# Kernel tuning notes

Hardware: AMD Instinct MI355X
Metric: run time of the kernel (lower is better)

The kernel has to match this reference:

```python
import jax, jax.numpy as jnp
import numpy as np

N_WORDS = 4096
N_HEADS = 512
EMB = 768          # input_size
HID = 1024         # hidden_size
DIST = 64          # dist_emb_size (forced by Conv1d(64, ...))
SENT_LEN = 64      # fixed sentence length -> static max padded length
PAIR_F = 2 * EMB + DIST  # 1600


def setup_inputs() -> dict:
    key = jax.random.key(0)
    ks = jax.random.split(key, 14)
    words = jax.random.normal(ks[0], (N_WORDS, EMB), dtype=jnp.float32)
    heads_ids = jax.random.randint(ks[1], (N_HEADS,), 0, N_WORDS, dtype=jnp.int64)
    sent_id = (jnp.arange(N_WORDS) // SENT_LEN).astype(jnp.int32)  # sorted, contiguous sentences
    s = 0.02
    return {
        "words": words,
        "heads_ids": heads_ids,
        "sent_id": sent_id,
        "emb_table": jax.random.normal(ks[2], (128, DIST), dtype=jnp.float32) * s,
        "W1": jax.random.normal(ks[3], (PAIR_F, HID), dtype=jnp.float32) * s,
        "b1": jnp.zeros((HID,), jnp.float32),
        "W2": jax.random.normal(ks[4], (HID, 256), dtype=jnp.float32) * s,
        "b2": jnp.zeros((256,), jnp.float32),
        "W3": jax.random.normal(ks[5], (256, DIST), dtype=jnp.float32) * s,
        "b3": jnp.zeros((DIST,), jnp.float32),
        "cw1": jax.random.normal(ks[6], (4, DIST, 3), dtype=jnp.float32) * s,  # Conv1d(64,4,3,1,1)
        "cb1": jnp.zeros((4,), jnp.float32),
        "cw2": jax.random.normal(ks[7], (2, 4, 3), dtype=jnp.float32) * s,    # Conv1d(4,2,3,1,1)
        "cb2": jnp.zeros((2,), jnp.float32),
    }


def _conv1d(x, w, b):
    # x: [N, C_in, L], w: [C_out, C_in, 3], padding=1, stride=1 (torch Conv1d semantics)
    y = jax.lax.conv_general_dilated(x, w, window_strides=(1,), padding=((1, 1),),
                                     dimension_numbers=("NCH", "OIH", "NCH"))
    return y + b[None, :, None]


def reference(words, heads_ids, sent_id, emb_table, W1, b1, W2, b2, W3, b3, cw1, cb1, cw2, cb2):
    n_words = words.shape[0]
    heads = heads_ids.astype(jnp.int32)
    H = heads.shape[0]

    # relative positions & distance-embedding ids, clamped to bucket 127 outside [-63, 63]
    rel = heads[:, None] - jnp.arange(n_words, dtype=jnp.int32)[None, :]      # [H, W]
    eid = rel + 63
    eid = jnp.where((eid < 0) | (eid > 126), 127, eid)

    # per-head sentence span (sent_id is sorted & contiguous)
    sh = sent_id[heads]
    starts = jnp.searchsorted(sent_id, sh, side="left")
    lengths = jnp.searchsorted(sent_id, sh, side="right") - starts            # [H]

    # padded ragged layout: row i holds words of head i's sentence, left-packed
    j = jnp.arange(SENT_LEN, dtype=jnp.int32)
    cols = starts[:, None] + j[None, :]                                       # [H, L]
    mask = j[None, :] < lengths[:, None]                                      # [H, L]
    cols_c = jnp.clip(cols, 0, n_words - 1)

    head_w = words[heads]                                                     # [H, E]
    col_w = words[cols_c]                                                     # [H, L, E]
    dist = emb_table[jnp.take_along_axis(eid, cols_c, axis=1)]                # [H, L, DIST]
    feat = jnp.concatenate(
        [jnp.broadcast_to(head_w[:, None, :], col_w.shape), col_w, dist], axis=-1)
    feat = jnp.where(mask[..., None], feat, jnp.zeros((), feat.dtype))        # zero padding rows (as torch)

    # FFNN (dropout is identity in eval mode)
    x = jax.nn.relu(feat @ W1 + b1)
    x = jax.nn.relu(x @ W2 + b2)
    x = x @ W3 + b3                                                           # [H, L, 64]

    # conv stack over the padded ragged axis
    x = _conv1d(x.transpose(0, 2, 1), cw1, cb1)
    x = _conv1d(x, cw2, cb2)
    res = x.transpose(0, 2, 1)                                                # [H, L, 2]

    # scatter back into [H, n_words, 2]; masked slots get out-of-range col -> dropped
    rows = jnp.broadcast_to(jnp.arange(H, dtype=jnp.int32)[:, None], mask.shape)
    cols_sc = jnp.where(mask, cols, n_words)
    scores = jnp.full((H, n_words, 2), -jnp.inf, dtype=words.dtype)
    scores = scores.at[rows, cols_sc].set(res, mode="drop")

    # eval-mode validity log-mask
    valid_starts = jnp.log((rel >= 0).astype(words.dtype))
    valid_ends = jnp.log((rel <= 0).astype(words.dtype))
    valid = jnp.stack([valid_starts, valid_ends], axis=2)
    return scores + valid
```

## Files before the change

kernel.cpp:

```cpp
#include <hip/hip_runtime.h>
#include <math.h>

#define NW   4096
#define NH   512
#define EMBD 768
#define HIDD 1024
#define DISTD 64
#define SLEN 64

#define NEG_BIG (-1.0e30f)

typedef __attribute__((ext_vector_type(8))) short short8;
typedef __attribute__((ext_vector_type(16))) float f32x16;
typedef __attribute__((ext_vector_type(4))) float f32x4;

#define MFMA32(a, b, c) __builtin_amdgcn_mfma_f32_32x32x16_bf16((a), (b), (c), 0, 0, 0)
#define MFMA16(a, b, c) __builtin_amdgcn_mfma_f32_16x16x32_bf16((a), (b), (c), 0, 0, 0)

__device__ __forceinline__ unsigned short f2bf(float f) {
    unsigned u = __float_as_uint(f);
    u += 0x7FFFu + ((u >> 16) & 1u);
    return (unsigned short)(u >> 16);
}
__device__ __forceinline__ float bf2f(unsigned short s) {
    return __uint_as_float(((unsigned)s) << 16);
}
__device__ __forceinline__ unsigned cvtpk(float lo, float hi) {
    unsigned r;
    asm("v_cvt_pk_bf16_f32 %0, %1, %2" : "=v"(r) : "v"(lo), "v"(hi));
    return r;
}
__device__ __forceinline__ short8 pack8(float f0, float f1, float f2, float f3,
                                        float f4, float f5, float f6, float f7) {
    union { unsigned u[4]; short8 s; } r;
    r.u[0] = cvtpk(f0, f1); r.u[1] = cvtpk(f2, f3);
    r.u[2] = cvtpk(f4, f5); r.u[3] = cvtpk(f6, f7);
    return r.s;
}

#define BARL()                                                   \
    do {                                                         \
        asm volatile("s_waitcnt lgkmcnt(0)" ::: "memory");       \
        __builtin_amdgcn_s_barrier();                            \
    } while (0)

__device__ __forceinline__ void pack_b32_dev(long t, const float* __restrict__ src,
                                             int ld, int nb32, int KB,
                                             unsigned short* __restrict__ dst)
{
    int l = (int)(t & 63); long u = t >> 6;
    int nb = (int)(u % nb32); int kb = (int)(u / nb32);
    int row0 = kb * 16 + ((l >> 5) << 3);
    int col  = (nb << 5) + (l & 31);
    const float* s = src + (size_t)row0 * ld + col;
    short8 v;
#pragma unroll
    for (int j = 0; j < 8; ++j) v[j] = (short)f2bf(s[(size_t)j * ld]);
    *(short8*)(dst + (((size_t)nb * KB + kb) << 9) + l * 8) = v;
}

__device__ __forceinline__ void pack_b16_dev(long t, const float* __restrict__ src,
                                             int ld, int nb16, int KB,
                                             unsigned short* __restrict__ dst)
{
    int l = (int)(t & 63); long u = t >> 6;
    int nb = (int)(u % nb16); int kb = (int)(u / nb16);
    int row0 = kb * 32 + ((l >> 4) << 3);
    int col  = (nb << 4) + (l & 15);
    const float* s = src + (size_t)row0 * ld + col;
    short8 v;
#pragma unroll
    for (int j = 0; j < 8; ++j) v[j] = (short)f2bf(s[(size_t)j * ld]);
    *(short8*)(dst + (((size_t)nb * KB + kb) << 9) + l * 8) = v;
}

__device__ __forceinline__ void cvt8_dev(long i, const float* __restrict__ src,
                                         unsigned short* __restrict__ dst)
{
    const float* s = src + i * 8;
    short8 v;
#pragma unroll
    for (int j = 0; j < 8; ++j) v[j] = (short)f2bf(s[j]);
    *(short8*)(dst + i * 8) = v;
}

#define WPS 776
__global__ __launch_bounds__(256)
void prep_kernel(const float* __restrict__ words, const float* __restrict__ emb,
                 const float* __restrict__ W1,
                 unsigned short* __restrict__ wpack, unsigned short* __restrict__ embb,
                 unsigned short* __restrict__ W1pa, unsigned short* __restrict__ W1px,
                 unsigned short* __restrict__ W1pd)
{
    __shared__ unsigned short tls[32 * WPS];

    const int b = blockIdx.x, tid = threadIdx.x;
    if (b < 128) {
        const int m = b;
#pragma unroll
        for (int i = 0; i < 24; ++i) {
            const int idx = tid + i * 256;
            const int r = idx / 192, c4 = (idx % 192) * 4;
            float4 v = *(const float4*)(words + ((size_t)(m * 32 + r)) * EMBD + c4);
            tls[r * WPS + c4 + 0] = f2bf(v.x);
            tls[r * WPS + c4 + 1] = f2bf(v.y);
            tls[r * WPS + c4 + 2] = f2bf(v.z);
            tls[r * WPS + c4 + 3] = f2bf(v.w);
        }
        __syncthreads();
        const int l = tid & 63, w = tid >> 6;
        for (int kb = w; kb < 48; kb += 4) {
            short8 v = *(const short8*)&tls[(l & 31) * WPS + kb * 16 + ((l >> 5) << 3)];
            *(short8*)(wpack + (((size_t)m * 48 + kb) << 9) + l * 8) = v;
        }
    } else if (b < 132) {
        cvt8_dev((long)(b - 128) * 256 + tid, emb, embb);
    } else if (b < 516) {
        pack_b32_dev((long)(b - 132) * 256 + tid, W1, HIDD, 32, 48, W1pa);
    } else if (b < 900) {
        pack_b32_dev((long)(b - 516) * 256 + tid, W1 + (size_t)768 * HIDD, HIDD, 32, 48, W1px);
    } else {
        pack_b32_dev((long)(b - 900) * 256 + tid, W1 + (size_t)1536 * HIDD, HIDD, 32, 4, W1pd);
    }
}

__global__ __launch_bounds__(256, 4)
void gemms_kernel(const unsigned short* __restrict__ wpack,
                  const unsigned short* __restrict__ embb,
                  const unsigned short* __restrict__ W1pa,
                  const unsigned short* __restrict__ W1px,
                  const unsigned short* __restrict__ W1pd,
                  const float* __restrict__ W2, const float* __restrict__ W3,
                  const float* __restrict__ b1, const int* __restrict__ heads,
                  const int* __restrict__ sent_id,
                  unsigned short* __restrict__ XwP, unsigned short* __restrict__ Hcb,
                  unsigned short* __restrict__ Dtb,
                  unsigned short* __restrict__ W2p, unsigned short* __restrict__ W3p,
                  int* __restrict__ starts, int* __restrict__ lens)
{
    __shared__ unsigned short tls[4][32 * 40];

    const int b = blockIdx.x, tid = threadIdx.x;
    const int l = tid & 63, w = tid >> 6;

    if (b < 1024) {
        const int mB = b >> 3, nB = b & 7;
        const int cbg = nB * 4 + w;
        const unsigned short* ap = wpack + (((size_t)mB * 48) << 9) + l * 8;
        const unsigned short* bp = W1px + (((size_t)cbg * 48) << 9) + l * 8;
        f32x16 acc = {};
#pragma unroll
        for (int kk = 0; kk < 48; ++kk) {
            short8 a = *(const short8*)(ap + ((size_t)kk << 9));
            short8 bb = *(const short8*)(bp + ((size_t)kk << 9));
            acc = MFMA32(a, bb, acc);
        }
        const int col = cbg * 32 + (l & 31);
        const float bv = b1[col];
        unsigned short* tw = tls[w];
#pragma unroll
        for (int r = 0; r < 16; ++r) {
            int rowl = (r & 3) + 8 * (r >> 2) + 4 * (l >> 5);
            tw[rowl * 40 + (l & 31)] = f2bf(acc[r] + bv);
        }
        short8 v0 = *(const short8*)&tw[(l & 31) * 40 + ((l >> 5) << 3)];
        short8 v1 = *(const short8*)&tw[(l & 31) * 40 + 16 + ((l >> 5) << 3)];
        *(short8*)(XwP + (((size_t)(mB * 64 + cbg * 2)) << 9) + l * 8) = v0;
        *(short8*)(XwP + (((size_t)(mB * 64 + cbg * 2 + 1)) << 9) + l * 8) = v1;
    } else if (b < 1152) {
        const int q = b - 1024;
        const int mB = q >> 3, nB = q & 7;
        const int cbg = nB * 4 + w;
        int row = heads[mB * 32 + (l & 31)];
        const unsigned short* ap = wpack + (((size_t)(row >> 5) * 48) << 9)
                                 + ((row & 31) + 32 * (l >> 5)) * 8;
        const unsigned short* bp = W1pa + (((size_t)cbg * 48) << 9) + l * 8;
        f32x16 acc = {};
#pragma unroll
        for (int kk = 0; kk < 48; ++kk) {
            short8 a = *(const short8*)(ap + ((size_t)kk << 9));
            short8 bb = *(const short8*)(bp + ((size_t)kk << 9));
            acc = MFMA32(a, bb, acc);
        }
        const int col = cbg * 32 + (l & 31);
#pragma unroll
        for (int r = 0; r < 16; ++r) {
            int rr = mB * 32 + (r & 3) + 8 * (r >> 2) + 4 * (l >> 5);
            Hcb[(size_t)rr * HIDD + col] = f2bf(acc[r]);
        }
    } else if (b < 1184) {
        const int q = b - 1152;
        const int mB = q >> 3, nB = q & 7;
        const int cbg = nB * 4 + w;
        const unsigned short* ap = embb + (size_t)(mB * 32 + (l & 31)) * DISTD + ((l >> 5) << 3);
        const unsigned short* bp = W1pd + (((size_t)cbg * 4) << 9) + l * 8;
        f32x16 acc = {};
#pragma unroll
        for (int kk = 0; kk < 4; ++kk) {
            short8 a = *(const short8*)(ap + kk * 16);
            short8 bb = *(const short8*)(bp + ((size_t)kk << 9));
            acc = MFMA32(a, bb, acc);
        }
        const int col = cbg * 32 + (l & 31);
#pragma unroll
        for (int r = 0; r < 16; ++r) {
            int rr = mB * 32 + (r & 3) + 8 * (r >> 2) + 4 * (l >> 5);
            Dtb[(size_t)rr * HIDD + col] = f2bf(acc[r]);
        }
    } else if (b < 1312) {
        pack_b32_dev((long)(b - 1184) * 256 + tid, W2, 256, 8, 64, W2p);
    } else if (b < 1320) {
        pack_b16_dev((long)(b - 1312) * 256 + tid, W3, 64, 4, 8, W3p);
    } else {
        int h = (b - 1320) * 256 + tid;
        if (h < NH) {
            int head = heads[h];
            int s = sent_id[head];
            int lo = 0, hi = NW;
            while (lo < hi) { int mid = (lo + hi) >> 1; if (sent_id[mid] < s) lo = mid + 1; else hi = mid; }
            int start = lo;
            lo = 0; hi = NW;
            while (lo < hi) { int mid = (lo + hi) >> 1; if (sent_id[mid] <= s) lo = mid + 1; else hi = mid; }
            int len = lo - start;
            if (len > SLEN) len = SLEN;
            starts[h] = start;
            lens[h] = len;
        }
    }
}

#define NT 32
__global__ __launch_bounds__(512)
void head_kernel(const unsigned short* __restrict__ XwP,
                 const unsigned short* __restrict__ Hcb,
                 const unsigned short* __restrict__ Dtb,
                 const unsigned short* __restrict__ W2p,
                 const float* __restrict__ b2,
                 const unsigned short* __restrict__ W3p,
                 const float* __restrict__ b3,
                 const float* __restrict__ cw1, const float* __restrict__ cb1,
                 const float* __restrict__ cw2, const float* __restrict__ cb2,
                 const int* __restrict__ heads, const int* __restrict__ starts,
                 const int* __restrict__ lens,
                 float* __restrict__ out)
{
    __shared__ char smem[67584];
    unsigned short* Ast = (unsigned short*)smem;
    unsigned short* Bst = (unsigned short*)(smem + 16384);
    unsigned short* x2s = (unsigned short*)smem;
    float* x3s = (float*)smem;
    float* y1s = (float*)(smem + 35328);
    float* y2s = (float*)(smem + 37376);

    const int tid = threadIdx.x;
    const int l = tid & 63, w = tid >> 6;
    const int h0 = blockIdx.x * 2;

    const int head0 = heads[h0],  head1 = heads[h0 + 1];
    const int strt0 = starts[h0], strt1 = starts[h0 + 1];
    const int len0  = lens[h0],   len1  = lens[h0 + 1];

    const int kkA = w >> 2, rb = w & 3;
    const int hbA = rb >> 1;
    const int headA = hbA ? head1 : head0;
    const int strtA = hbA ? strt1 : strt0;
    const int q0A = 63 - (headA - strtA);
    const unsigned short* xwPp =
        XwP + (((size_t)((strtA >> 5) + (rb & 1)) * 64) << 9) + l * 8;
    const int ddRow = 126 - q0A - 32 * (rb & 1) - (l & 31);
    const unsigned short* ddPp = Dtb + (size_t)ddRow * HIDD + ((l >> 5) << 3);
    const unsigned short* hcp = Hcb + (size_t)(h0 + hbA) * HIDD + ((l >> 5) << 3);
    const int kkB = w >> 2, nbB0 = (w & 3) * 2;
    const int mb = w & 1, nq = w >> 1;

    f32x16 acc[2][2] = {};

    short8 rxw, rhc, rdd, rb0, rb1;

#define LOADT(t)                                                              \
    {                                                                         \
        const int kb_ = (t) * 2 + kkA;                                        \
        rxw = *(const short8*)(xwPp + ((size_t)kb_ << 9));                    \
        rdd = *(const short8*)(ddPp + kb_ * 16);                              \
        rhc = *(const short8*)(hcp + kb_ * 16);                               \
        const size_t c0_ = ((size_t)(nbB0 * 64 + (t) * 2 + kkB)) << 9;        \
        rb0 = *(const short8*)(W2p + c0_ + l * 8);                            \
        rb1 = *(const short8*)(W2p + c0_ + 32768 + l * 8);                    \
    }

#define WRITET(t)                                                             \
    {                                                                         \
        const int buf_ = (t) & 1;                                             \
        float f_[8];                                                          \
        _Pragma("unroll")                                                     \
        for (int j = 0; j < 8; ++j)                                           \
            f_[j] = fmaxf(bf2f((unsigned short)rxw[j])                        \
                        + bf2f((unsigned short)rhc[j])                        \
                        + bf2f((unsigned short)rdd[j]), 0.f);                 \
        short8 v_ = pack8(f_[0], f_[1], f_[2], f_[3], f_[4], f_[5], f_[6], f_[7]); \
        *(short8*)&Ast[buf_ * 4096 + (kkA * 4 + rb) * 512 + l * 8] = v_;      \
        *(short8*)&Bst[buf_ * 8192 + (kkB * 8 + nbB0) * 512 + l * 8] = rb0;   \
        *(short8*)&Bst[buf_ * 8192 + (kkB * 8 + nbB0 + 1) * 512 + l * 8] = rb1; \
    }

    LOADT(0);
    WRITET(0);
    LOADT(1);
    BARL();

#pragma unroll 2
    for (int t = 0; t < NT; ++t) {
        const int buf = t & 1;
        short8 af0[2], af1[2], bf0[2], bf1[2];
#pragma unroll
        for (int k2 = 0; k2 < 2; ++k2) {
            af0[k2] = *(const short8*)&Ast[buf * 4096 + (k2 * 4 + mb * 2 + 0) * 512 + l * 8];
            af1[k2] = *(const short8*)&Ast[buf * 4096 + (k2 * 4 + mb * 2 + 1) * 512 + l * 8];
            bf0[k2] = *(const short8*)&Bst[buf * 8192 + (k2 * 8 + nq * 2 + 0) * 512 + l * 8];
            bf1[k2] = *(const short8*)&Bst[buf * 8192 + (k2 * 8 + nq * 2 + 1) * 512 + l * 8];
        }
        if (t + 1 < NT) WRITET(t + 1);
        if (t + 2 < NT) LOADT(t + 2);
#pragma unroll
        for (int k2 = 0; k2 < 2; ++k2) {
            acc[0][0] = MFMA32(af0[k2], bf0[k2], acc[0][0]);
            acc[0][1] = MFMA32(af0[k2], bf1[k2], acc[0][1]);
            acc[1][0] = MFMA32(af1[k2], bf0[k2], acc[1][0]);
            acc[1][1] = MFMA32(af1[k2], bf1[k2], acc[1][1]);
        }
        BARL();
    }

#pragma unroll
    for (int i = 0; i < 2; ++i) {
#pragma unroll
        for (int n = 0; n < 2; ++n) {
            const int ct = nq * 64 + n * 32 + (l & 31);
            const float bv = b2[ct];
#pragma unroll
            for (int r = 0; r < 16; ++r) {
                const int rt = mb * 64 + i * 32 + (r & 3) + 8 * (r >> 2) + 4 * (l >> 5);
                const int hb = rt >> 6, rl = rt & 63;
                x2s[hb * 16896 + rl * 264 + ct] = f2bf(fmaxf(acc[i][n][r] + bv, 0.f));
            }
        }
    }
    __syncthreads();

    {
        const int hb = w >> 2, q = w & 3;
        const unsigned short* x2h = x2s + hb * 16896;
        f32x4 acc2[4] = {};
#pragma unroll
        for (int kk = 0; kk < 8; ++kk) {
            short8 bf = *(const short8*)(W3p + ((q * 8 + kk) << 9) + l * 8);
#pragma unroll
            for (int mi = 0; mi < 4; ++mi) {
                short8 af = *(const short8*)&x2h[(mi * 16 + (l & 15)) * 264 + kk * 32 + ((l >> 4) << 3)];
                acc2[mi] = MFMA16(af, bf, acc2[mi]);
            }
        }
        __syncthreads();
        float* x3h = x3s + hb * 4416;
        const int col = q * 16 + (l & 15);
        const float b3v = b3[col];
#pragma unroll
        for (int mi = 0; mi < 4; ++mi) {
#pragma unroll
            for (int r = 0; r < 4; ++r) {
                const int rowv = mi * 16 + (l >> 4) * 4 + r;
                x3h[rowv * 69 + col] = acc2[mi][r] + b3v;
            }
        }
    }
    __syncthreads();

    {
        const int hb3 = tid >> 8;
        const int co = (tid >> 6) & 3;
        const int ll = tid & 63;
        const float* x3h = x3s + hb3 * 4416;
        float s = cb1[co];
        const float* wb = cw1 + co * DISTD * 3;
        for (int ci = 0; ci < DISTD; ++ci) {
            float w0 = wb[ci * 3 + 0], w1 = wb[ci * 3 + 1], w2v = wb[ci * 3 + 2];
            float xm = (ll > 0) ? x3h[(ll - 1) * 69 + ci] : 0.f;
            float xc = x3h[ll * 69 + ci];
            float xp = (ll < 63) ? x3h[(ll + 1) * 69 + ci] : 0.f;
            s = fmaf(xm, w0, s);
            s = fmaf(xc, w1, s);
            s = fmaf(xp, w2v, s);
        }
        y1s[hb3 * 256 + co * 64 + ll] = s;
    }
    __syncthreads();

    if (tid < 256) {
        const int hb4 = tid >> 7;
        const int co = (tid >> 6) & 1;
        const int ll = tid & 63;
        const float* yh = y1s + hb4 * 256;
        const int head = hb4 ? head1 : head0;
        const int strt = hb4 ? strt1 : strt0;
        float s = cb2[co];
#pragma unroll
        for (int ci = 0; ci < 4; ++ci) {
            const float* wb = cw2 + (co * 4 + ci) * 3;
            const float* yr = yh + ci * 64;
            float xm = (ll > 0) ? yr[ll - 1] : 0.f;
            float xc = yr[ll];
            float xp = (ll < 63) ? yr[ll + 1] : 0.f;
            s = fmaf(xm, wb[0], s);
            s = fmaf(xc, wb[1], s);
            s = fmaf(xp, wb[2], s);
        }
        const int col = strt + ll;
        const int rel = head - col;
        const bool valid = (co == 0) ? (rel >= 0) : (rel <= 0);
        y2s[hb4 * 128 + ll * 2 + co] = valid ? s : NEG_BIG;
    }
    __syncthreads();

    {
        const int hb = tid >> 8;
        const int c8 = tid & 255;
        const int strt = hb ? strt1 : strt0;
        const int len  = hb ? len1  : len0;
        float* orow = out + ((size_t)(h0 + hb) * NW) * 2;
        const float* yh = y2s + hb * 128;
#pragma unroll
        for (int i = 0; i < 16; ++i) {
            const int col = i * 256 + c8;
            float2 v;
            if (col >= strt && col < strt + len) {
                v = *(const float2*)&yh[(col - strt) * 2];
            } else {
                v.x = NEG_BIG; v.y = NEG_BIG;
            }
            *(float2*)&orow[(size_t)col * 2] = v;
        }
    }
}

extern "C" void kernel_launch(void* const* d_in, const int* in_sizes, int n_in,
                              void* d_out, int out_size, void* d_ws, size_t ws_size,
                              hipStream_t stream)
{
    const float* words = (const float*)d_in[0];
    const int* heads   = (const int*)d_in[1];
    const int* sent_id = (const int*)d_in[2];
    const float* emb   = (const float*)d_in[3];
    const float* W1    = (const float*)d_in[4];
    const float* b1    = (const float*)d_in[5];
    const float* W2    = (const float*)d_in[6];
    const float* b2    = (const float*)d_in[7];
    const float* W3    = (const float*)d_in[8];
    const float* b3    = (const float*)d_in[9];
    const float* cw1   = (const float*)d_in[10];
    const float* cb1   = (const float*)d_in[11];
    const float* cw2   = (const float*)d_in[12];
    const float* cb2   = (const float*)d_in[13];
    float* out = (float*)d_out;

    char* wsb = (char*)d_ws;
    unsigned short* XwP  = (unsigned short*)(wsb + 0);
    unsigned short* Hcb  = (unsigned short*)(wsb + 8388608);
    unsigned short* Dtb  = (unsigned short*)(wsb + 9437184);
    unsigned short* W2p  = (unsigned short*)(wsb + 9699328);
    unsigned short* W3p  = (unsigned short*)(wsb + 10223616);
    unsigned short* embb = (unsigned short*)(wsb + 10256384);
    int* starts          = (int*)(wsb + 10272768);
    int* lens            = (int*)(wsb + 10274816);
    char* ob = (char*)d_out;
    unsigned short* wpack  = (unsigned short*)(ob + 0);
    unsigned short* W1pa   = (unsigned short*)(ob + 6291456);
    unsigned short* W1px   = (unsigned short*)(ob + 7864320);
    unsigned short* W1pd   = (unsigned short*)(ob + 9437184);
    (void)ws_size; (void)in_sizes; (void)n_in; (void)out_size;

    prep_kernel<<<dim3(932), dim3(256), 0, stream>>>(
        words, emb, W1, wpack, embb, W1pa, W1px, W1pd);

    gemms_kernel<<<dim3(1322), dim3(256), 0, stream>>>(
        wpack, embb, W1pa, W1px, W1pd, W2, W3, b1, heads, sent_id,
        XwP, Hcb, Dtb, W2p, W3p, starts, lens);

    head_kernel<<<dim3(NH / 2), dim3(512), 0, stream>>>(
        XwP, Hcb, Dtb, W2p, b2, W3p, b3, cw1, cb1, cw2, cb2,
        heads, starts, lens, out);
}
```

Measured before the change: 73.67 us.

## Load W2 fragments directly into registers instead of staging through LDS

The W2 operand of the second GEMM is now read from global memory straight into per-wave register fragments, double-buffered two k-steps ahead, instead of being cooperatively loaded, written to shared memory and read back. This removes the LDS writes and reads for B and halves the shared-memory traffic per tile. In exchange, each wave fetches its own B fragments, so warps sharing the same columns load redundant copies from global/L2, and more registers are held live for the prefetched fragments.

```diff
diff --git a/kernel.cpp b/kernel.cpp
--- a/kernel.cpp
+++ b/kernel.cpp
@@ -246,7 +246,6 @@
 {
     __shared__ char smem[67584];
     unsigned short* Ast = (unsigned short*)smem;
-    unsigned short* Bst = (unsigned short*)(smem + 16384);
     unsigned short* x2s = (unsigned short*)smem;
     float* x3s = (float*)smem;
     float* y1s = (float*)(smem + 35328);
@@ -270,25 +269,25 @@
     const int ddRow = 126 - q0A - 32 * (rb & 1) - (l & 31);
     const unsigned short* ddPp = Dtb + (size_t)ddRow * HIDD + ((l >> 5) << 3);
     const unsigned short* hcp = Hcb + (size_t)(h0 + hbA) * HIDD + ((l >> 5) << 3);
-    const int kkB = w >> 2, nbB0 = (w & 3) * 2;
     const int mb = w & 1, nq = w >> 1;
+    const unsigned short* bp0 = W2p + (((size_t)(nq * 2) * 64) << 9) + l * 8;
+    const unsigned short* bp1 = W2p + (((size_t)(nq * 2 + 1) * 64) << 9) + l * 8;
 
     f32x16 acc[2][2] = {};
 
-    short8 rxw, rhc, rdd, rb0, rb1;
-
-#define LOADT(t)                                                              \
+    short8 rxw, rhc, rdd;
+    short8 sA00, sA01, sA10, sA11;
+    short8 sB00, sB01, sB10, sB11;
+
+#define LOADA(t)                                                              \
     {                                                                         \
         const int kb_ = (t) * 2 + kkA;                                        \
         rxw = *(const short8*)(xwPp + ((size_t)kb_ << 9));                    \
         rdd = *(const short8*)(ddPp + kb_ * 16);                              \
         rhc = *(const short8*)(hcp + kb_ * 16);                               \
-        const size_t c0_ = ((size_t)(nbB0 * 64 + (t) * 2 + kkB)) << 9;        \
-        rb0 = *(const short8*)(W2p + c0_ + l * 8);                            \
-        rb1 = *(const short8*)(W2p + c0_ + 32768 + l * 8);                    \
-    }
-
-#define WRITET(t)                                                             \
+    }
+
+#define WRITEA(t)                                                             \
     {                                                                         \
         const int buf_ = (t) & 1;                                             \
         float f_[8];                                                          \
@@ -299,35 +298,50 @@
                         + bf2f((unsigned short)rdd[j]), 0.f);                 \
         short8 v_ = pack8(f_[0], f_[1], f_[2], f_[3], f_[4], f_[5], f_[6], f_[7]); \
         *(short8*)&Ast[buf_ * 4096 + (kkA * 4 + rb) * 512 + l * 8] = v_;      \
-        *(short8*)&Bst[buf_ * 8192 + (kkB * 8 + nbB0) * 512 + l * 8] = rb0;   \
-        *(short8*)&Bst[buf_ * 8192 + (kkB * 8 + nbB0 + 1) * 512 + l * 8] = rb1; \
-    }
-
-    LOADT(0);
-    WRITET(0);
-    LOADT(1);
+    }
+
+#define LOADB(t, B00, B01, B10, B11)                                          \
+    {                                                                         \
+        const int kb0_ = (t) * 2;                                             \
+        B00 = *(const short8*)(bp0 + ((size_t)kb0_ << 9));                    \
+        B01 = *(const short8*)(bp1 + ((size_t)kb0_ << 9));                    \
+        B10 = *(const short8*)(bp0 + ((size_t)(kb0_ + 1) << 9));              \
+        B11 = *(const short8*)(bp1 + ((size_t)(kb0_ + 1) << 9));              \
+    }
+
+#define MFMA_STEP(buf_, B00, B01, B10, B11)                                   \
+    {                                                                         \
+        short8 af0_0 = *(const short8*)&Ast[(buf_) * 4096 + (mb * 2 + 0) * 512 + l * 8]; \
+        short8 af1_0 = *(const short8*)&Ast[(buf_) * 4096 + (mb * 2 + 1) * 512 + l * 8]; \
+        short8 af0_1 = *(const short8*)&Ast[(buf_) * 4096 + (4 + mb * 2 + 0) * 512 + l * 8]; \
+        short8 af1_1 = *(const short8*)&Ast[(buf_) * 4096 + (4 + mb * 2 + 1) * 512 + l * 8]; \
+        acc[0][0] = MFMA32(af0_0, B00, acc[0][0]);                            \
+        acc[0][1] = MFMA32(af0_0, B01, acc[0][1]);                            \
+        acc[1][0] = MFMA32(af1_0, B00, acc[1][0]);                            \
+        acc[1][1] = MFMA32(af1_0, B01, acc[1][1]);                            \
+        acc[0][0] = MFMA32(af0_1, B10, acc[0][0]);                            \
+        acc[0][1] = MFMA32(af0_1, B11, acc[0][1]);                            \
+        acc[1][0] = MFMA32(af1_1, B10, acc[1][0]);                            \
+        acc[1][1] = MFMA32(af1_1, B11, acc[1][1]);                            \
+    }
+
+    LOADA(0);
+    WRITEA(0);
+    LOADA(1);
+    LOADB(0, sA00, sA01, sA10, sA11);
+    LOADB(1, sB00, sB01, sB10, sB11);
     BARL();
 
-#pragma unroll 2
-    for (int t = 0; t < NT; ++t) {
-        const int buf = t & 1;
-        short8 af0[2], af1[2], bf0[2], bf1[2];
-#pragma unroll
-        for (int k2 = 0; k2 < 2; ++k2) {
-            af0[k2] = *(const short8*)&Ast[buf * 4096 + (k2 * 4 + mb * 2 + 0) * 512 + l * 8];
-            af1[k2] = *(const short8*)&Ast[buf * 4096 + (k2 * 4 + mb * 2 + 1) * 512 + l * 8];
-            bf0[k2] = *(const short8*)&Bst[buf * 8192 + (k2 * 8 + nq * 2 + 0) * 512 + l * 8];
-            bf1[k2] = *(const short8*)&Bst[buf * 8192 + (k2 * 8 + nq * 2 + 1) * 512 + l * 8];
-        }
-        if (t + 1 < NT) WRITET(t + 1);
-        if (t + 2 < NT) LOADT(t + 2);
-#pragma unroll
-        for (int k2 = 0; k2 < 2; ++k2) {
-            acc[0][0] = MFMA32(af0[k2], bf0[k2], acc[0][0]);
-            acc[0][1] = MFMA32(af0[k2], bf1[k2], acc[0][1]);
-            acc[1][0] = MFMA32(af1[k2], bf0[k2], acc[1][0]);
-            acc[1][1] = MFMA32(af1[k2], bf1[k2], acc[1][1]);
-        }
+    for (int t = 0; t < NT; t += 2) {
+        if (t + 1 < NT) WRITEA(t + 1);
+        if (t + 2 < NT) LOADA(t + 2);
+        MFMA_STEP(0, sA00, sA01, sA10, sA11);
+        if (t + 2 < NT) LOADB(t + 2, sA00, sA01, sA10, sA11);
+        BARL();
+        if (t + 2 < NT) WRITEA(t + 2);
+        if (t + 3 < NT) LOADA(t + 3);
+        MFMA_STEP(1, sB00, sB01, sB10, sB11);
+        if (t + 3 < NT) LOADB(t + 3, sB00, sB01, sB10, sB11);
         BARL();
     }
 
```

New measurement: 79.75 us. 1.08x slower.
